# Kernel optimization log

Hardware: AMD Instinct MI355X
Metric: run time of the kernel (lower is better)

The kernel has to match this reference:

```python
import jax, jax.numpy as jnp
import numpy as np

N_NODES = 50000
N_EDGES = 800000
IN_DIM = 89
HID = 128
N_CLASSES = 64
N_GRAPHS = 64


def setup_inputs() -> dict:
    key = jax.random.key(0)
    ks = jax.random.split(key, 12)
    nf = jax.random.normal(ks[0], (N_NODES, IN_DIM), dtype=jnp.float32)
    src = jax.random.randint(ks[1], (N_EDGES,), 0, N_NODES, dtype=jnp.int32)
    dst = jnp.sort(jax.random.randint(ks[2], (N_EDGES,), 0, N_NODES, dtype=jnp.int32))
    graph_id = jnp.sort(jax.random.randint(ks[3], (N_NODES,), 0, N_GRAPHS, dtype=jnp.int32))
    s = 0.05
    W1 = jax.random.normal(ks[4], (IN_DIM, HID), dtype=jnp.float32) * s
    b1 = jnp.zeros((HID,), jnp.float32)
    W2 = jax.random.normal(ks[5], (HID, HID), dtype=jnp.float32) * s
    b2 = jnp.zeros((HID,), jnp.float32)
    W3 = jax.random.normal(ks[6], (HID, HID), dtype=jnp.float32) * s
    b3 = jnp.zeros((HID,), jnp.float32)
    Wc1 = jax.random.normal(ks[7], (HID, HID), dtype=jnp.float32) * s
    bc1 = jnp.zeros((HID,), jnp.float32)
    Wc2 = jax.random.normal(ks[8], (HID, N_CLASSES), dtype=jnp.float32) * s
    bc2 = jnp.zeros((N_CLASSES,), jnp.float32)
    return {"nf": nf, "src": src, "dst": dst, "graph_id": graph_id,
            "n_graphs": N_GRAPHS,
            "W1": W1, "b1": b1, "W2": W2, "b2": b2, "W3": W3, "b3": b3,
            "Wc1": Wc1, "bc1": bc1, "Wc2": Wc2, "bc2": bc2}


def reference(nf, src, dst, graph_id, n_graphs, W1, b1, W2, b2, W3, b3, Wc1, bc1, Wc2, bc2):
    n = nf.shape[0]
    # in-degree per destination node (DGL mean over mailbox); clamp to avoid /0
    deg = jax.ops.segment_sum(jnp.ones((src.shape[0],), nf.dtype), dst, num_segments=n)
    inv_deg = (1.0 / jnp.maximum(deg, 1.0))[:, None]

    def gcn(h, W, b):
        # copy_u: gather source features per edge, mean-reduce by dst, linear+ReLU
        agg = jax.ops.segment_sum(h[src], dst, num_segments=n) * inv_deg
        return jax.nn.relu(agg @ W + b)

    h = gcn(nf, W1, b1)
    h = gcn(h, W2, b2)
    h = gcn(h, W3, b3)

    # dgl.mean_nodes: per-graph mean pool over nodes
    cnt = jax.ops.segment_sum(jnp.ones((n,), h.dtype), graph_id, num_segments=n_graphs)
    hg = jax.ops.segment_sum(h, graph_id, num_segments=n_graphs) / jnp.maximum(cnt, 1.0)[:, None]

    return jax.nn.relu(hg @ Wc1 + bc1) @ Wc2 + bc2
```

## Files before the change

### kernel.cpp

```cpp
#include <hip/hip_runtime.h>

#define N_NODES   50000
#define N_EDGES   800000
#define IN_DIM    89
#define KP1       96
#define HID       128
#define N_CLASSES 64
#define N_GRAPHS  64
#define PSPLIT    16

typedef __attribute__((ext_vector_type(8))) short bf16x8;
typedef __attribute__((ext_vector_type(4))) float f32x4;

__device__ __forceinline__ unsigned short f2bf(float x) {
    union { float f; unsigned u; } v; v.f = x;
    unsigned r = v.u + 0x7FFF + ((v.u >> 16) & 1);
    return (unsigned short)(r >> 16);
}
__device__ __forceinline__ float bf2f(unsigned short x) {
    union { unsigned u; float f; } v; v.u = ((unsigned)x) << 16;
    return v.f;
}

#define NB_CONV 18750
#define NB_ROW  196
#define NB_WT   176

__global__ void prep_kernel(const float* __restrict__ nf,
                            const int* __restrict__ dst,
                            const int* __restrict__ gid,
                            const float* __restrict__ W1,
                            const float* __restrict__ W2,
                            const float* __restrict__ W3,
                            unsigned short* __restrict__ nfb,
                            int* __restrict__ node_ptr,
                            int* __restrict__ graph_ptr,
                            unsigned short* __restrict__ wt1,
                            unsigned short* __restrict__ wt2,
                            unsigned short* __restrict__ wt3) {
    const int b = blockIdx.x;
    if (b < NB_CONV) {
        const int i = b * 256 + threadIdx.x;
        const int row = i / KP1, k = i - row * KP1;
        nfb[i] = (k < IN_DIM) ? f2bf(nf[(size_t)row * IN_DIM + k]) : (unsigned short)0;
    } else if (b < NB_CONV + NB_ROW) {
        const int i = (b - NB_CONV) * 256 + threadIdx.x;
        if (i <= N_NODES) {
            int lo = 0, hi = N_EDGES;
            while (lo < hi) { int mid = (lo + hi) >> 1; if (dst[mid] < i) lo = mid + 1; else hi = mid; }
            node_ptr[i] = lo;
        }
        if (i <= N_GRAPHS) {
            int lo = 0, hi = N_NODES;
            while (lo < hi) { int mid = (lo + hi) >> 1; if (gid[mid] < i) lo = mid + 1; else hi = mid; }
            graph_ptr[i] = lo;
        }
    } else {
        int idx = (b - NB_CONV - NB_ROW) * 256 + threadIdx.x;
        if (idx < HID * KP1) {
            const int col = idx / KP1, k = idx - col * KP1;
            wt1[idx] = (k < IN_DIM) ? f2bf(W1[(size_t)k * HID + col]) : (unsigned short)0;
        } else if ((idx -= HID * KP1) < HID * HID) {
            const int col = idx / HID, k = idx - col * HID;
            wt2[idx] = f2bf(W2[(size_t)k * HID + col]);
        } else if ((idx -= HID * HID) < HID * HID) {
            const int col = idx / HID, k = idx - col * HID;
            wt3[idx] = f2bf(W3[(size_t)k * HID + col]);
        }
    }
}

template <int KPAD>
__global__ __launch_bounds__(256) void mfma_gemm_kernel(
        const unsigned short* __restrict__ Xb,
        const unsigned short* __restrict__ WT,
        unsigned short* __restrict__ Y, int M) {
    const int wave = threadIdx.x >> 6;
    const int lane = threadIdx.x & 63;
    const int r    = lane & 15;
    const int kg   = lane >> 4;

    const int row  = blockIdx.x * 64 + wave * 16 + r;
    const int rowc = (row < M) ? row : (M - 1);

    f32x4 acc[8];
#pragma unroll
    for (int i = 0; i < 8; ++i) acc[i] = (f32x4){0.f, 0.f, 0.f, 0.f};

    const unsigned short* xrow = Xb + (size_t)rowc * KPAD + kg * 8;

#pragma unroll
    for (int k0 = 0; k0 < KPAD; k0 += 32) {
        const bf16x8 a = *reinterpret_cast<const bf16x8*>(xrow + k0);
#pragma unroll
        for (int nf = 0; nf < 8; ++nf) {
            const bf16x8 b = *reinterpret_cast<const bf16x8*>(
                WT + (size_t)(nf * 16 + r) * KPAD + kg * 8 + k0);
            acc[nf] = __builtin_amdgcn_mfma_f32_16x16x32_bf16(a, b, acc[nf], 0, 0, 0);
        }
    }

    const int orow0 = blockIdx.x * 64 + wave * 16 + kg * 4;
#pragma unroll
    for (int nf = 0; nf < 8; ++nf)
#pragma unroll
        for (int q = 0; q < 4; ++q) {
            const int orow = orow0 + q;
            if (orow < M) Y[(size_t)orow * HID + nf * 16 + r] = f2bf(acc[nf][q]);
        }
}

__global__ __launch_bounds__(256) void fused_agg_gemm_kernel(
        const unsigned short* __restrict__ Pin,
        const int* __restrict__ src,
        const int* __restrict__ node_ptr,
        const float* __restrict__ bias,
        const unsigned short* __restrict__ WT,
        unsigned short* __restrict__ Pout) {
    __shared__ unsigned short hs[16][136];

    const int wave = threadIdx.x >> 6;
    const int lane = threadIdx.x & 63;
    const int q    = lane >> 4;
    const int g    = lane & 15;
    const int vbase = blockIdx.x * 16;

    const float4 b0 = *reinterpret_cast<const float4*>(bias + g * 8);
    const float4 b1 = *reinterpret_cast<const float4*>(bias + g * 8 + 4);

#pragma unroll
    for (int i = 0; i < 4; ++i) {
        const int li = wave * 4 + i;
        const int v  = vbase + li;
        const int lo = node_ptr[v];
        const int hi = node_ptr[v + 1];
        const float inv = 1.0f / (float)max(hi - lo, 1);

        float acc[8];
#pragma unroll
        for (int j = 0; j < 8; ++j) acc[j] = 0.f;

        int e = lo + q;
        for (; e + 4 < hi; e += 8) {
            const int u0 = src[e];
            const int u1 = src[e + 4];
            const bf16x8 r0 = *reinterpret_cast<const bf16x8*>(Pin + (size_t)u0 * HID + g * 8);
            const bf16x8 r1 = *reinterpret_cast<const bf16x8*>(Pin + (size_t)u1 * HID + g * 8);
#pragma unroll
            for (int j = 0; j < 8; ++j)
                acc[j] += bf2f((unsigned short)r0[j]) + bf2f((unsigned short)r1[j]);
        }
        if (e < hi) {
            const int u = src[e];
            const bf16x8 r = *reinterpret_cast<const bf16x8*>(Pin + (size_t)u * HID + g * 8);
#pragma unroll
            for (int j = 0; j < 8; ++j) acc[j] += bf2f((unsigned short)r[j]);
        }
#pragma unroll
        for (int j = 0; j < 8; ++j) {
            acc[j] += __shfl_xor(acc[j], 16);
            acc[j] += __shfl_xor(acc[j], 32);
        }
        if (q == 0) {
            bf16x8 ob;
            ob[0] = (short)f2bf(fmaxf(acc[0] * inv + b0.x, 0.f));
            ob[1] = (short)f2bf(fmaxf(acc[1] * inv + b0.y, 0.f));
            ob[2] = (short)f2bf(fmaxf(acc[2] * inv + b0.z, 0.f));
            ob[3] = (short)f2bf(fmaxf(acc[3] * inv + b0.w, 0.f));
            ob[4] = (short)f2bf(fmaxf(acc[4] * inv + b1.x, 0.f));
            ob[5] = (short)f2bf(fmaxf(acc[5] * inv + b1.y, 0.f));
            ob[6] = (short)f2bf(fmaxf(acc[6] * inv + b1.z, 0.f));
            ob[7] = (short)f2bf(fmaxf(acc[7] * inv + b1.w, 0.f));
            *reinterpret_cast<bf16x8*>(&hs[li][g * 8]) = ob;
        }
    }
    __syncthreads();

    const int r  = lane & 15;
    const int kg = lane >> 4;

    f32x4 acc2[2];
#pragma unroll
    for (int t = 0; t < 2; ++t) acc2[t] = (f32x4){0.f, 0.f, 0.f, 0.f};

#pragma unroll
    for (int k0 = 0; k0 < HID; k0 += 32) {
        const bf16x8 a = *reinterpret_cast<const bf16x8*>(&hs[r][kg * 8 + k0]);
#pragma unroll
        for (int t = 0; t < 2; ++t) {
            const int nf = wave * 2 + t;
            const bf16x8 b = *reinterpret_cast<const bf16x8*>(
                WT + (size_t)(nf * 16 + r) * HID + kg * 8 + k0);
            acc2[t] = __builtin_amdgcn_mfma_f32_16x16x32_bf16(a, b, acc2[t], 0, 0, 0);
        }
    }

    const int orow0 = vbase + kg * 4;
#pragma unroll
    for (int t = 0; t < 2; ++t) {
        const int nf = wave * 2 + t;
#pragma unroll
        for (int p = 0; p < 4; ++p)
            Pout[(size_t)(orow0 + p) * HID + nf * 16 + r] = f2bf(acc2[t][p]);
    }
}

__global__ void agg128_f32_kernel(const unsigned short* __restrict__ Pb,
                                  const int* __restrict__ src,
                                  const int* __restrict__ node_ptr,
                                  const float* __restrict__ bias,
                                  float* __restrict__ out) {
    const int wave = threadIdx.x >> 6;
    const int lane = threadIdx.x & 63;
    const int v    = blockIdx.x * 4 + wave;
    if (v >= N_NODES) return;

    const int lo = node_ptr[v];
    const int hi = node_ptr[v + 1];
    const float inv = 1.0f / (float)max(hi - lo, 1);

    const int q = lane >> 4;
    const int g = lane & 15;

    float acc[8];
#pragma unroll
    for (int j = 0; j < 8; ++j) acc[j] = 0.f;

    int e = lo + q;
    for (; e + 4 < hi; e += 8) {
        const int u0 = src[e];
        const int u1 = src[e + 4];
        const bf16x8 r0 = *reinterpret_cast<const bf16x8*>(Pb + (size_t)u0 * HID + g * 8);
        const bf16x8 r1 = *reinterpret_cast<const bf16x8*>(Pb + (size_t)u1 * HID + g * 8);
#pragma unroll
        for (int j = 0; j < 8; ++j)
            acc[j] += bf2f((unsigned short)r0[j]) + bf2f((unsigned short)r1[j]);
    }
    if (e < hi) {
        const int u = src[e];
        const bf16x8 r = *reinterpret_cast<const bf16x8*>(Pb + (size_t)u * HID + g * 8);
#pragma unroll
        for (int j = 0; j < 8; ++j) acc[j] += bf2f((unsigned short)r[j]);
    }
#pragma unroll
    for (int j = 0; j < 8; ++j) {
        acc[j] += __shfl_xor(acc[j], 16);
        acc[j] += __shfl_xor(acc[j], 32);
    }

    if (q == 0) {
        const float4 b0 = *reinterpret_cast<const float4*>(bias + g * 8);
        const float4 b1 = *reinterpret_cast<const float4*>(bias + g * 8 + 4);
        float4 a = make_float4(fmaxf(acc[0] * inv + b0.x, 0.f), fmaxf(acc[1] * inv + b0.y, 0.f),
                               fmaxf(acc[2] * inv + b0.z, 0.f), fmaxf(acc[3] * inv + b0.w, 0.f));
        float4 b = make_float4(fmaxf(acc[4] * inv + b1.x, 0.f), fmaxf(acc[5] * inv + b1.y, 0.f),
                               fmaxf(acc[6] * inv + b1.z, 0.f), fmaxf(acc[7] * inv + b1.w, 0.f));
        *reinterpret_cast<float4*>(out + (size_t)v * HID + g * 8)     = a;
        *reinterpret_cast<float4*>(out + (size_t)v * HID + g * 8 + 4) = b;
    }
}

__global__ void pool_partial_kernel(const float* __restrict__ h3,
                                    const int* __restrict__ graph_ptr,
                                    float* __restrict__ hgp) {
    const int g   = blockIdx.x / PSPLIT;
    const int s   = blockIdx.x % PSPLIT;
    const int j   = threadIdx.x;
    const int lo  = graph_ptr[g];
    const int hi  = graph_ptr[g + 1];

    float acc = 0.f;
    for (int r = lo + s; r < hi; r += PSPLIT)
        acc += h3[(size_t)r * HID + j];
    hgp[(size_t)blockIdx.x * HID + j] = acc;
}

__global__ void cls_kernel(const float* __restrict__ hgp,
                           const int* __restrict__ graph_ptr,
                           const float* __restrict__ Wc1,
                           const float* __restrict__ bc1,
                           const float* __restrict__ Wc2,
                           const float* __restrict__ bc2,
                           float* __restrict__ out) {
    const int g = blockIdx.x;
    const int j = threadIdx.x;
    const int cnt = graph_ptr[g + 1] - graph_ptr[g];
    const float inv = 1.0f / (float)max(cnt, 1);

    float acc = 0.f;
#pragma unroll
    for (int s = 0; s < PSPLIT; ++s)
        acc += hgp[(size_t)(g * PSPLIT + s) * HID + j];

    __shared__ float row[HID];
    __shared__ float trow[HID];
    row[j] = acc * inv;
    __syncthreads();

    float a1 = bc1[j];
#pragma unroll 4
    for (int k = 0; k < HID; ++k) a1 = fmaf(row[k], Wc1[k * HID + j], a1);
    trow[j] = fmaxf(a1, 0.f);
    __syncthreads();

    if (j < N_CLASSES) {
        float a2 = bc2[j];
#pragma unroll 4
        for (int k = 0; k < HID; ++k) a2 = fmaf(trow[k], Wc2[k * N_CLASSES + j], a2);
        out[g * N_CLASSES + j] = a2;
    }
}

extern "C" void kernel_launch(void* const* d_in, const int* in_sizes, int n_in,
                              void* d_out, int out_size, void* d_ws, size_t ws_size,
                              hipStream_t stream) {
    const float* nf   = (const float*)d_in[0];
    const int*   src  = (const int*)  d_in[1];
    const int*   dst  = (const int*)  d_in[2];
    const int*   gid  = (const int*)  d_in[3];
    const float* W1  = (const float*)d_in[5];
    const float* b1  = (const float*)d_in[6];
    const float* W2  = (const float*)d_in[7];
    const float* b2  = (const float*)d_in[8];
    const float* W3  = (const float*)d_in[9];
    const float* b3  = (const float*)d_in[10];
    const float* Wc1 = (const float*)d_in[11];
    const float* bc1 = (const float*)d_in[12];
    const float* Wc2 = (const float*)d_in[13];
    const float* bc2 = (const float*)d_in[14];
    float* out = (float*)d_out;

    char* ws = (char*)d_ws;
    size_t off = 0;
    auto alloc = [&](size_t bytes) { void* p = ws + off; off = (off + bytes + 255) & ~(size_t)255; return p; };
    int*   node_ptr  = (int*)  alloc((N_NODES + 1) * sizeof(int));
    int*   graph_ptr = (int*)  alloc((N_GRAPHS + 1) * sizeof(int));
    char*  regionA   = (char*) alloc((size_t)N_NODES * HID * sizeof(float));
    unsigned short* nfb = (unsigned short*)regionA;
    float*          h3  = (float*)regionA;
    unsigned short* PbA = (unsigned short*)alloc((size_t)N_NODES * HID * sizeof(unsigned short));
    unsigned short* PbB = (unsigned short*)alloc((size_t)N_NODES * HID * sizeof(unsigned short));
    unsigned short* wt1 = (unsigned short*)alloc((size_t)HID * KP1 * sizeof(unsigned short));
    unsigned short* wt2 = (unsigned short*)alloc((size_t)HID * HID * sizeof(unsigned short));
    unsigned short* wt3 = (unsigned short*)alloc((size_t)HID * HID * sizeof(unsigned short));
    float* hgp       = (float*)alloc((size_t)N_GRAPHS * PSPLIT * HID * sizeof(float));
    (void)ws_size;

    const int GEMM_GRID  = (N_NODES + 63) / 64;
    const int FUSED_GRID = N_NODES / 16;
    const int AGG_GRID   = (N_NODES + 3) / 4;

    prep_kernel<<<NB_CONV + NB_ROW + NB_WT, 256, 0, stream>>>(
        nf, dst, gid, W1, W2, W3, nfb, node_ptr, graph_ptr, wt1, wt2, wt3);

    mfma_gemm_kernel<KP1><<<GEMM_GRID, 256, 0, stream>>>(nfb, wt1, PbA, N_NODES);

    fused_agg_gemm_kernel<<<FUSED_GRID, 256, 0, stream>>>(PbA, src, node_ptr, b1, wt2, PbB);

    fused_agg_gemm_kernel<<<FUSED_GRID, 256, 0, stream>>>(PbB, src, node_ptr, b2, wt3, PbA);

    agg128_f32_kernel<<<AGG_GRID, 256, 0, stream>>>(PbA, src, node_ptr, b3, h3);

    pool_partial_kernel<<<N_GRAPHS * PSPLIT, HID, 0, stream>>>(h3, graph_ptr, hgp);
    cls_kernel<<<N_GRAPHS, HID, 0, stream>>>(hgp, graph_ptr, Wc1, bc1, Wc2, bc2, out);
}
```

Measured before the change: 179.6 us.

## Fuse nf bf16 conversion into first GEMM, widen fused kernel, unroll gathers

```diff
diff --git a/kernel.cpp b/kernel.cpp
--- a/kernel.cpp
+++ b/kernel.cpp
@@ -22,29 +22,22 @@
     return v.f;
 }
 
-#define NB_CONV 18750
 #define NB_ROW  196
 #define NB_WT   176
 
-__global__ void prep_kernel(const float* __restrict__ nf,
-                            const int* __restrict__ dst,
+__global__ void prep_kernel(const int* __restrict__ dst,
                             const int* __restrict__ gid,
                             const float* __restrict__ W1,
                             const float* __restrict__ W2,
                             const float* __restrict__ W3,
-                            unsigned short* __restrict__ nfb,
                             int* __restrict__ node_ptr,
                             int* __restrict__ graph_ptr,
                             unsigned short* __restrict__ wt1,
                             unsigned short* __restrict__ wt2,
                             unsigned short* __restrict__ wt3) {
     const int b = blockIdx.x;
-    if (b < NB_CONV) {
+    if (b < NB_ROW) {
         const int i = b * 256 + threadIdx.x;
-        const int row = i / KP1, k = i - row * KP1;
-        nfb[i] = (k < IN_DIM) ? f2bf(nf[(size_t)row * IN_DIM + k]) : (unsigned short)0;
-    } else if (b < NB_CONV + NB_ROW) {
-        const int i = (b - NB_CONV) * 256 + threadIdx.x;
         if (i <= N_NODES) {
             int lo = 0, hi = N_EDGES;
             while (lo < hi) { int mid = (lo + hi) >> 1; if (dst[mid] < i) lo = mid + 1; else hi = mid; }
@@ -56,7 +49,7 @@
             graph_ptr[i] = lo;
         }
     } else {
-        int idx = (b - NB_CONV - NB_ROW) * 256 + threadIdx.x;
+        int idx = (b - NB_ROW) * 256 + threadIdx.x;
         if (idx < HID * KP1) {
             const int col = idx / KP1, k = idx - col * KP1;
             wt1[idx] = (k < IN_DIM) ? f2bf(W1[(size_t)k * HID + col]) : (unsigned short)0;
@@ -70,9 +63,8 @@
     }
 }
 
-template <int KPAD>
-__global__ __launch_bounds__(256) void mfma_gemm_kernel(
-        const unsigned short* __restrict__ Xb,
+__global__ __launch_bounds__(256) void gemm1_kernel(
+        const float* __restrict__ nf,
         const unsigned short* __restrict__ WT,
         unsigned short* __restrict__ Y, int M) {
     const int wave = threadIdx.x >> 6;
@@ -83,41 +75,52 @@
     const int row  = blockIdx.x * 64 + wave * 16 + r;
     const int rowc = (row < M) ? row : (M - 1);
 
+    bf16x8 afrag[3];
+#pragma unroll
+    for (int t = 0; t < 3; ++t) {
+        const int kb = 32 * t + kg * 8;
+#pragma unroll
+        for (int j = 0; j < 8; ++j) {
+            const int k = kb + j;
+            const float v = (k < IN_DIM) ? nf[(size_t)rowc * IN_DIM + k] : 0.f;
+            afrag[t][j] = (short)f2bf(v);
+        }
+    }
+
     f32x4 acc[8];
 #pragma unroll
     for (int i = 0; i < 8; ++i) acc[i] = (f32x4){0.f, 0.f, 0.f, 0.f};
 
-    const unsigned short* xrow = Xb + (size_t)rowc * KPAD + kg * 8;
-
-#pragma unroll
-    for (int k0 = 0; k0 < KPAD; k0 += 32) {
-        const bf16x8 a = *reinterpret_cast<const bf16x8*>(xrow + k0);
-#pragma unroll
-        for (int nf = 0; nf < 8; ++nf) {
+#pragma unroll
+    for (int t = 0; t < 3; ++t) {
+        const int k0 = 32 * t;
+#pragma unroll
+        for (int c = 0; c < 8; ++c) {
             const bf16x8 b = *reinterpret_cast<const bf16x8*>(
-                WT + (size_t)(nf * 16 + r) * KPAD + kg * 8 + k0);
-            acc[nf] = __builtin_amdgcn_mfma_f32_16x16x32_bf16(a, b, acc[nf], 0, 0, 0);
+                WT + (size_t)(c * 16 + r) * KP1 + kg * 8 + k0);
+            acc[c] = __builtin_amdgcn_mfma_f32_16x16x32_bf16(afrag[t], b, acc[c], 0, 0, 0);
         }
     }
 
     const int orow0 = blockIdx.x * 64 + wave * 16 + kg * 4;
 #pragma unroll
-    for (int nf = 0; nf < 8; ++nf)
-#pragma unroll
-        for (int q = 0; q < 4; ++q) {
-            const int orow = orow0 + q;
-            if (orow < M) Y[(size_t)orow * HID + nf * 16 + r] = f2bf(acc[nf][q]);
-        }
-}
-
-__global__ __launch_bounds__(256) void fused_agg_gemm_kernel(
+    for (int c = 0; c < 8; ++c)
+#pragma unroll
+        for (int p = 0; p < 4; ++p) {
+            const int orow = orow0 + p;
+            if (orow < M) Y[(size_t)orow * HID + c * 16 + r] = f2bf(acc[c][p]);
+        }
+}
+
+#define HS_STRIDE 140
+__global__ __launch_bounds__(512) void fused_agg_gemm_kernel(
         const unsigned short* __restrict__ Pin,
         const int* __restrict__ src,
         const int* __restrict__ node_ptr,
         const float* __restrict__ bias,
         const unsigned short* __restrict__ WT,
         unsigned short* __restrict__ Pout) {
-    __shared__ unsigned short hs[16][136];
+    __shared__ unsigned short hs[16 * HS_STRIDE];
 
     const int wave = threadIdx.x >> 6;
     const int lane = threadIdx.x & 63;
@@ -129,8 +132,8 @@
     const float4 b1 = *reinterpret_cast<const float4*>(bias + g * 8 + 4);
 
 #pragma unroll
-    for (int i = 0; i < 4; ++i) {
-        const int li = wave * 4 + i;
+    for (int i = 0; i < 2; ++i) {
+        const int li = wave * 2 + i;
         const int v  = vbase + li;
         const int lo = node_ptr[v];
         const int hi = node_ptr[v + 1];
@@ -141,16 +144,21 @@
         for (int j = 0; j < 8; ++j) acc[j] = 0.f;
 
         int e = lo + q;
-        for (; e + 4 < hi; e += 8) {
+        for (; e + 12 < hi; e += 16) {
             const int u0 = src[e];
             const int u1 = src[e + 4];
+            const int u2 = src[e + 8];
+            const int u3 = src[e + 12];
             const bf16x8 r0 = *reinterpret_cast<const bf16x8*>(Pin + (size_t)u0 * HID + g * 8);
             const bf16x8 r1 = *reinterpret_cast<const bf16x8*>(Pin + (size_t)u1 * HID + g * 8);
+            const bf16x8 r2 = *reinterpret_cast<const bf16x8*>(Pin + (size_t)u2 * HID + g * 8);
+            const bf16x8 r3 = *reinterpret_cast<const bf16x8*>(Pin + (size_t)u3 * HID + g * 8);
 #pragma unroll
             for (int j = 0; j < 8; ++j)
-                acc[j] += bf2f((unsigned short)r0[j]) + bf2f((unsigned short)r1[j]);
-        }
-        if (e < hi) {
+                acc[j] += (bf2f((unsigned short)r0[j]) + bf2f((unsigned short)r1[j]))
+                        + (bf2f((unsigned short)r2[j]) + bf2f((unsigned short)r3[j]));
+        }
+        for (; e < hi; e += 4) {
             const int u = src[e];
             const bf16x8 r = *reinterpret_cast<const bf16x8*>(Pin + (size_t)u * HID + g * 8);
 #pragma unroll
@@ -171,7 +179,7 @@
             ob[5] = (short)f2bf(fmaxf(acc[5] * inv + b1.y, 0.f));
             ob[6] = (short)f2bf(fmaxf(acc[6] * inv + b1.z, 0.f));
             ob[7] = (short)f2bf(fmaxf(acc[7] * inv + b1.w, 0.f));
-            *reinterpret_cast<bf16x8*>(&hs[li][g * 8]) = ob;
+            *reinterpret_cast<bf16x8*>(&hs[li * HS_STRIDE + g * 8]) = ob;
         }
     }
     __syncthreads();
@@ -179,30 +187,19 @@
     const int r  = lane & 15;
     const int kg = lane >> 4;
 
-    f32x4 acc2[2];
-#pragma unroll
-    for (int t = 0; t < 2; ++t) acc2[t] = (f32x4){0.f, 0.f, 0.f, 0.f};
-
+    f32x4 acc2 = (f32x4){0.f, 0.f, 0.f, 0.f};
 #pragma unroll
     for (int k0 = 0; k0 < HID; k0 += 32) {
-        const bf16x8 a = *reinterpret_cast<const bf16x8*>(&hs[r][kg * 8 + k0]);
-#pragma unroll
-        for (int t = 0; t < 2; ++t) {
-            const int nf = wave * 2 + t;
-            const bf16x8 b = *reinterpret_cast<const bf16x8*>(
-                WT + (size_t)(nf * 16 + r) * HID + kg * 8 + k0);
-            acc2[t] = __builtin_amdgcn_mfma_f32_16x16x32_bf16(a, b, acc2[t], 0, 0, 0);
-        }
+        const bf16x8 a = *reinterpret_cast<const bf16x8*>(&hs[r * HS_STRIDE + kg * 8 + k0]);
+        const bf16x8 b = *reinterpret_cast<const bf16x8*>(
+            WT + (size_t)(wave * 16 + r) * HID + kg * 8 + k0);
+        acc2 = __builtin_amdgcn_mfma_f32_16x16x32_bf16(a, b, acc2, 0, 0, 0);
     }
 
     const int orow0 = vbase + kg * 4;
 #pragma unroll
-    for (int t = 0; t < 2; ++t) {
-        const int nf = wave * 2 + t;
-#pragma unroll
-        for (int p = 0; p < 4; ++p)
-            Pout[(size_t)(orow0 + p) * HID + nf * 16 + r] = f2bf(acc2[t][p]);
-    }
+    for (int p = 0; p < 4; ++p)
+        Pout[(size_t)(orow0 + p) * HID + wave * 16 + r] = f2bf(acc2[p]);
 }
 
 __global__ void agg128_f32_kernel(const unsigned short* __restrict__ Pb,
@@ -227,16 +224,21 @@
     for (int j = 0; j < 8; ++j) acc[j] = 0.f;
 
     int e = lo + q;
-    for (; e + 4 < hi; e += 8) {
+    for (; e + 12 < hi; e += 16) {
         const int u0 = src[e];
         const int u1 = src[e + 4];
+        const int u2 = src[e + 8];
+        const int u3 = src[e + 12];
         const bf16x8 r0 = *reinterpret_cast<const bf16x8*>(Pb + (size_t)u0 * HID + g * 8);
         const bf16x8 r1 = *reinterpret_cast<const bf16x8*>(Pb + (size_t)u1 * HID + g * 8);
+        const bf16x8 r2 = *reinterpret_cast<const bf16x8*>(Pb + (size_t)u2 * HID + g * 8);
+        const bf16x8 r3 = *reinterpret_cast<const bf16x8*>(Pb + (size_t)u3 * HID + g * 8);
 #pragma unroll
         for (int j = 0; j < 8; ++j)
-            acc[j] += bf2f((unsigned short)r0[j]) + bf2f((unsigned short)r1[j]);
-    }
-    if (e < hi) {
+            acc[j] += (bf2f((unsigned short)r0[j]) + bf2f((unsigned short)r1[j]))
+                    + (bf2f((unsigned short)r2[j]) + bf2f((unsigned short)r3[j]));
+    }
+    for (; e < hi; e += 4) {
         const int u = src[e];
         const bf16x8 r = *reinterpret_cast<const bf16x8*>(Pb + (size_t)u * HID + g * 8);
 #pragma unroll
@@ -335,9 +337,7 @@
     auto alloc = [&](size_t bytes) { void* p = ws + off; off = (off + bytes + 255) & ~(size_t)255; return p; };
     int*   node_ptr  = (int*)  alloc((N_NODES + 1) * sizeof(int));
     int*   graph_ptr = (int*)  alloc((N_GRAPHS + 1) * sizeof(int));
-    char*  regionA   = (char*) alloc((size_t)N_NODES * HID * sizeof(float));
-    unsigned short* nfb = (unsigned short*)regionA;
-    float*          h3  = (float*)regionA;
+    float* h3        = (float*)alloc((size_t)N_NODES * HID * sizeof(float));
     unsigned short* PbA = (unsigned short*)alloc((size_t)N_NODES * HID * sizeof(unsigned short));
     unsigned short* PbB = (unsigned short*)alloc((size_t)N_NODES * HID * sizeof(unsigned short));
     unsigned short* wt1 = (unsigned short*)alloc((size_t)HID * KP1 * sizeof(unsigned short));
@@ -350,14 +350,14 @@
     const int FUSED_GRID = N_NODES / 16;
     const int AGG_GRID   = (N_NODES + 3) / 4;
 
-    prep_kernel<<<NB_CONV + NB_ROW + NB_WT, 256, 0, stream>>>(
-        nf, dst, gid, W1, W2, W3, nfb, node_ptr, graph_ptr, wt1, wt2, wt3);
-
-    mfma_gemm_kernel<KP1><<<GEMM_GRID, 256, 0, stream>>>(nfb, wt1, PbA, N_NODES);
-
-    fused_agg_gemm_kernel<<<FUSED_GRID, 256, 0, stream>>>(PbA, src, node_ptr, b1, wt2, PbB);
-
-    fused_agg_gemm_kernel<<<FUSED_GRID, 256, 0, stream>>>(PbB, src, node_ptr, b2, wt3, PbA);
+    prep_kernel<<<NB_ROW + NB_WT, 256, 0, stream>>>(
+        dst, gid, W1, W2, W3, node_ptr, graph_ptr, wt1, wt2, wt3);
+
+    gemm1_kernel<<<GEMM_GRID, 256, 0, stream>>>(nf, wt1, PbA, N_NODES);
+
+    fused_agg_gemm_kernel<<<FUSED_GRID, 512, 0, stream>>>(PbA, src, node_ptr, b1, wt2, PbB);
+
+    fused_agg_gemm_kernel<<<FUSED_GRID, 512, 0, stream>>>(PbB, src, node_ptr, b2, wt3, PbA);
 
     agg128_f32_kernel<<<AGG_GRID, 256, 0, stream>>>(PbA, src, node_ptr, b3, h3);
 
```

Result: no change. 179.9 us (+0.1%).
